# Kernel optimization log

Hardware: AMD Instinct MI355X
Metric: run time of the kernel (lower is better)

Reference implementation:

```python
import jax, jax.numpy as jnp
import numpy as np

B, S, HID = 4, 2048, 576
NH, NKV, HD = 9, 3, 64
MAXPOS, THETA = 8192, 100000.0


def rotate_half(x):
    x1, x2 = x[..., : x.shape[-1] // 2], x[..., x.shape[-1] // 2 :]
    return jnp.concatenate((-x2, x1), axis=-1)


def setup_inputs() -> dict:
    key = jax.random.key(0)
    ks = jax.random.split(key, 6)
    x = jax.random.normal(ks[0], (B, S, HID), dtype=jnp.float32)
    # RoPE tables (HuggingFace layout: freqs duplicated across halves)
    inv_freq = 1.0 / (THETA ** (np.arange(0, HD, 2, dtype=np.float32) / HD))
    freqs = np.outer(np.arange(MAXPOS, dtype=np.float32), inv_freq)
    emb = np.concatenate([freqs, freqs], axis=-1)
    cos = jnp.asarray(np.cos(emb))
    sin = jnp.asarray(np.sin(emb))
    position_ids = jnp.broadcast_to(jnp.arange(S, dtype=jnp.int64), (B, S))
    # additive causal mask [B,1,S,S]
    causal = jnp.where(
        jnp.tril(jnp.ones((S, S), dtype=bool)), 0.0, -1e9
    ).astype(jnp.float32)
    attention_mask = jnp.broadcast_to(causal, (B, 1, S, S))
    scale = 0.02
    wq = jax.random.normal(ks[1], (NH * HD, HID), dtype=jnp.float32) * scale
    wk = jax.random.normal(ks[2], (NKV * HD, HID), dtype=jnp.float32) * scale
    wv = jax.random.normal(ks[3], (NKV * HD, HID), dtype=jnp.float32) * scale
    wo = jax.random.normal(ks[4], (HID, NH * HD), dtype=jnp.float32) * scale
    return {
        "x": x, "cos": cos, "sin": sin, "position_ids": position_ids,
        "attention_mask": attention_mask,
        "wq": wq, "wk": wk, "wv": wv, "wo": wo,
    }


def reference(x, cos, sin, position_ids, attention_mask, wq, wk, wv, wo):
    b, s, _ = x.shape
    # projections (nn.Linear: y = x @ W.T), split into heads -> [B,H,S,D]
    q = (x @ wq.T).reshape(b, s, NH, HD).transpose(0, 2, 1, 3)
    k = (x @ wk.T).reshape(b, s, NKV, HD).transpose(0, 2, 1, 3)
    v = (x @ wv.T).reshape(b, s, NKV, HD).transpose(0, 2, 1, 3)
    # RoPE: cos/sin gathered per position -> [B,1,S,D], broadcast over heads
    c = cos[position_ids][:, None, :, :]
    si = sin[position_ids][:, None, :, :]
    q = q * c + rotate_half(q) * si
    k = k * c + rotate_half(k) * si
    # GQA expansion: repeat_interleave kv heads to match q heads
    k = jnp.repeat(k, NH // NKV, axis=1)
    v = jnp.repeat(v, NH // NKV, axis=1)
    scale = 1.0 / jnp.sqrt(jnp.asarray(HD, dtype=x.dtype))
    scores = jnp.einsum("bhqd,bhkd->bhqk", q, k) * scale + attention_mask
    attn = jax.nn.softmax(scores.astype(jnp.float32), axis=-1).astype(q.dtype)
    out = jnp.einsum("bhqk,bhkd->bhqd", attn, v)
    out = out.transpose(0, 2, 1, 3).reshape(b, s, NH * HD)
    return out @ wo.T
```

## Files before the change

kernel.cpp:

```cpp
#include <hip/hip_runtime.h>
#include <hip/hip_bf16.h>

#define B_    4
#define S_    2048
#define HID_  576
#define NH_   9
#define NKV_  3
#define HD_   64
#define GQ_   3

typedef __attribute__((ext_vector_type(8))) short bf16x8;
typedef __attribute__((ext_vector_type(4))) float f32x4;

__device__ __forceinline__ short f2bf(float f) {
    union { float f; unsigned int u; } v; v.f = f;
    unsigned int r = (v.u + 0x7fffu + ((v.u >> 16) & 1u)) >> 16;
    return (short)r;
}

__device__ __forceinline__ int pk2(float lo, float hi) {
    union { __hip_bfloat162 h; int u; } v;
    v.h = __float22bfloat162_rn(make_float2(lo, hi));
    return v.u;
}

__device__ __forceinline__ float exp2fast(float x) {
    return __builtin_amdgcn_exp2f(x);
}

__device__ __forceinline__ void async16(const void* g, void* l) {
    __builtin_amdgcn_global_load_lds(
        (const __attribute__((address_space(1))) unsigned int*)g,
        (__attribute__((address_space(3))) unsigned int*)l, 16, 0, 0);
}

__global__ __launch_bounds__(256) void qkv_kernel(
    const float* __restrict__ x,
    const float* __restrict__ wq,
    const float* __restrict__ wk,
    const float* __restrict__ wv,
    const float* __restrict__ cosb,
    const float* __restrict__ sinb,
    short* __restrict__ Q,
    short* __restrict__ K,
    short* __restrict__ Vt)
{
    __shared__ __align__(16) short As[2][256 * 64];
    __shared__ __align__(16) short Bs[2][64 * 64];

    const int m0     = blockIdx.x * 256;
    const int nb_blk = blockIdx.y;
    const int tid  = threadIdx.x;
    const int w    = tid >> 6, lane = tid & 63;
    const int quad = lane >> 4, c = lane & 15;
    const int lr   = lane >> 3, lg = lane & 7;
    const int sw   = lg ^ lr;
    const int xg   = quad ^ (c & 7);

    int type, head;
    if (nb_blk < NH_)            { type = 0; head = nb_blk; }
    else if (nb_blk < NH_ + NKV_){ type = 1; head = nb_blk - NH_; }
    else                         { type = 2; head = nb_blk - NH_ - NKV_; }
    const float* wsrc = (type == 0) ? wq + (size_t)head * 64 * HID_
                      : (type == 1) ? wk + (size_t)head * 64 * HID_
                                    : wv + (size_t)head * 64 * HID_;

    f32x4 acc[4][4];
    #pragma unroll
    for (int mt = 0; mt < 4; ++mt)
        #pragma unroll
        for (int nb = 0; nb < 4; ++nb) acc[mt][nb] = (f32x4){0.f, 0.f, 0.f, 0.f};

    float4 la[8][2], lb[2][2];
    auto load_stage = [&](int step) {
        const int k0 = step * 64;
        #pragma unroll
        for (int r = 0; r < 8; ++r) {
            int ch = w * 8 + r, R = ch * 8 + lr;
            const float* s = x + (size_t)(m0 + R) * HID_ + k0 + sw * 8;
            la[r][0] = *(const float4*)s;
            la[r][1] = *(const float4*)(s + 4);
        }
        #pragma unroll
        for (int r = 0; r < 2; ++r) {
            int ch = w * 2 + r, R = ch * 8 + lr;
            const float* s = wsrc + (size_t)R * HID_ + k0 + sw * 8;
            lb[r][0] = *(const float4*)s;
            lb[r][1] = *(const float4*)(s + 4);
        }
    };
    auto write_stage = [&](short* dstA, short* dstB) {
        #pragma unroll
        for (int r = 0; r < 8; ++r) {
            int ch = w * 8 + r;
            int4 p = { pk2(la[r][0].x, la[r][0].y), pk2(la[r][0].z, la[r][0].w),
                       pk2(la[r][1].x, la[r][1].y), pk2(la[r][1].z, la[r][1].w) };
            *(int4*)((char*)dstA + ch * 1024 + lane * 16) = p;
        }
        #pragma unroll
        for (int r = 0; r < 2; ++r) {
            int ch = w * 2 + r;
            int4 p = { pk2(lb[r][0].x, lb[r][0].y), pk2(lb[r][0].z, lb[r][0].w),
                       pk2(lb[r][1].x, lb[r][1].y), pk2(lb[r][1].z, lb[r][1].w) };
            *(int4*)((char*)dstB + ch * 1024 + lane * 16) = p;
        }
    };

    load_stage(0);
    write_stage(As[0], Bs[0]);

    int buf = 0;
    for (int kk = 0; kk < 9; ++kk) {
        __syncthreads();
        if (kk < 8) load_stage(kk + 1);

        const short* a_s = As[buf];
        const short* b_s = Bs[buf];
        bf16x8 bfr[4][2];
        #pragma unroll
        for (int nb = 0; nb < 4; ++nb) {
            int row = nb * 16 + c;
            bfr[nb][0] = *(const bf16x8*)(b_s + row * 64 + xg * 8);
            bfr[nb][1] = *(const bf16x8*)(b_s + row * 64 + (xg ^ 4) * 8);
        }
        #pragma unroll
        for (int mt = 0; mt < 4; ++mt) {
            int row = w * 64 + mt * 16 + c;
            bf16x8 a0 = *(const bf16x8*)(a_s + row * 64 + xg * 8);
            bf16x8 a1 = *(const bf16x8*)(a_s + row * 64 + (xg ^ 4) * 8);
            #pragma unroll
            for (int nb = 0; nb < 4; ++nb) {
                acc[mt][nb] = __builtin_amdgcn_mfma_f32_16x16x32_bf16(a0, bfr[nb][0], acc[mt][nb], 0, 0, 0);
                acc[mt][nb] = __builtin_amdgcn_mfma_f32_16x16x32_bf16(a1, bfr[nb][1], acc[mt][nb], 0, 0, 0);
            }
        }
        if (kk < 8) write_stage(As[buf ^ 1], Bs[buf ^ 1]);
        buf ^= 1;
    }

    const int b  = m0 >> 11;
    const int s0 = m0 & (S_ - 1);

    if (type < 2) {
        const float qs = (type == 0) ? 0.18033688f : 1.0f;
        #pragma unroll
        for (int mt = 0; mt < 4; ++mt)
            #pragma unroll
            for (int reg = 0; reg < 4; ++reg) {
                int s = s0 + w * 64 + mt * 16 + quad * 4 + reg;
                const float* cr = cosb + (size_t)s * HD_;
                const float* sr = sinb + (size_t)s * HD_;
                float a0 = acc[mt][0][reg], a1 = acc[mt][1][reg];
                float a2 = acc[mt][2][reg], a3 = acc[mt][3][reg];
                float o0 = (a0 * cr[c]      - a2 * sr[c])      * qs;
                float o1 = (a1 * cr[c + 16] - a3 * sr[c + 16]) * qs;
                float o2 = (a2 * cr[c + 32] + a0 * sr[c + 32]) * qs;
                float o3 = (a3 * cr[c + 48] + a1 * sr[c + 48]) * qs;
                short* dst = (type == 0)
                    ? Q + (((size_t)b * NH_  + head) * S_ + s) * HD_
                    : K + (((size_t)b * NKV_ + head) * S_ + s) * HD_;
                dst[c]      = f2bf(o0);
                dst[c + 16] = f2bf(o1);
                dst[c + 32] = f2bf(o2);
                dst[c + 48] = f2bf(o3);
            }
    } else {
        short* base = Vt + (((size_t)b * NKV_ + head) * HD_) * S_;
        #pragma unroll
        for (int mt = 0; mt < 4; ++mt) {
            int s4 = s0 + w * 64 + mt * 16 + quad * 4;
            #pragma unroll
            for (int nb = 0; nb < 4; ++nb) {
                int d = nb * 16 + c;
                short4 pk = make_short4(f2bf(acc[mt][nb][0]), f2bf(acc[mt][nb][1]),
                                        f2bf(acc[mt][nb][2]), f2bf(acc[mt][nb][3]));
                *(short4*)(base + (size_t)d * S_ + s4) = pk;
            }
        }
    }
}

#define PSTR 72

__global__ __launch_bounds__(256) void attn_kernel(
    const short* __restrict__ Q,
    const short* __restrict__ K,
    const short* __restrict__ Vt,
    short* __restrict__ AOb)
{
    __shared__ __align__(16) short Ks[2][64 * 64];
    __shared__ __align__(16) short Vs[2][64 * 64];
    __shared__ __align__(16) short Ps[3][64 * PSTR];

    const int bk = blockIdx.x;
    const int b  = bk / 3, kh = bk % 3;
    const int qt = 31 - blockIdx.y;
    const int tid  = threadIdx.x;
    const int w    = tid >> 6, lane = tid & 63;
    const int quad = lane >> 4, c = lane & 15;
    const int lr   = lane >> 3, lg = lane & 7;
    const int sw   = lg ^ lr;
    const int xg   = quad ^ (c & 7);

    const short* Kg = K  + (((size_t)b * NKV_ + kh) * S_) * HD_;
    const short* Vg = Vt + (((size_t)b * NKV_ + kh) * HD_) * S_;

    #pragma unroll
    for (int r = 0; r < 4; ++r) {
        int it = w * 4 + r;
        if (it < 8) {
            int R = it * 8 + lr;
            async16(Kg + (size_t)R * HD_ + sw * 8, (char*)Ks[0] + it * 1024);
        } else {
            int R = (it - 8) * 8 + lr;
            async16(Vg + (size_t)R * S_ + sw * 8, (char*)Vs[0] + (it - 8) * 1024);
        }
    }

    bf16x8 aq[3][2];
    #pragma unroll
    for (int hh = 0; hh < 3; ++hh) {
        const short* Qg = Q + (((size_t)b * NH_ + kh * GQ_ + hh) * S_ + qt * 64) * HD_;
        const short* qrow = Qg + (size_t)(w * 16 + c) * HD_;
        aq[hh][0] = *(const bf16x8*)(qrow + quad * 8);
        aq[hh][1] = *(const bf16x8*)(qrow + 32 + quad * 8);
    }

    bf16x8 ones;
    #pragma unroll
    for (int i = 0; i < 8; ++i) ones[i] = (short)0x3F80;

    f32x4 acc_o[3][4];
    #pragma unroll
    for (int hh = 0; hh < 3; ++hh)
        #pragma unroll
        for (int dt = 0; dt < 4; ++dt) acc_o[hh][dt] = (f32x4){0.f, 0.f, 0.f, 0.f};
    f32x4 acc_l[3] = { (f32x4){0.f,0.f,0.f,0.f}, (f32x4){0.f,0.f,0.f,0.f},
                       (f32x4){0.f,0.f,0.f,0.f} };

    auto do_tile = [&](const short* ks, const short* vs, bool MASK) {
        #pragma unroll
        for (int nb = 0; nb < 4; ++nb) {
            bf16x8 bk0 = *(const bf16x8*)(ks + (nb * 16 + c) * 64 + xg * 8);
            bf16x8 bk1 = *(const bf16x8*)(ks + (nb * 16 + c) * 64 + (xg ^ 4) * 8);
            #pragma unroll
            for (int hh = 0; hh < 3; ++hh) {
                f32x4 z = (f32x4){0.f, 0.f, 0.f, 0.f};
                z = __builtin_amdgcn_mfma_f32_16x16x32_bf16(aq[hh][0], bk0, z, 0, 0, 0);
                z = __builtin_amdgcn_mfma_f32_16x16x32_bf16(aq[hh][1], bk1, z, 0, 0, 0);
                #pragma unroll
                for (int r = 0; r < 4; ++r) {
                    float sv = z[r] - 4.0f;
                    if (MASK && (nb * 16 + c > w * 16 + quad * 4 + r)) sv = -1e30f;
                    Ps[hh][(w * 16 + quad * 4 + r) * PSTR + nb * 16 + c] = f2bf(exp2fast(sv));
                }
            }
        }
        #pragma unroll
        for (int kc = 0; kc < 2; ++kc) {
            int pg = kc ? (xg ^ 4) : xg;
            bf16x8 bv[4];
            #pragma unroll
            for (int dt = 0; dt < 4; ++dt)
                bv[dt] = *(const bf16x8*)(vs + (dt * 16 + c) * 64 + pg * 8);
            #pragma unroll
            for (int hh = 0; hh < 3; ++hh) {
                bf16x8 ap = *(const bf16x8*)(Ps[hh] + (w * 16 + c) * PSTR
                                             + quad * 8 + kc * 32);
                #pragma unroll
                for (int dt = 0; dt < 4; ++dt)
                    acc_o[hh][dt] = __builtin_amdgcn_mfma_f32_16x16x32_bf16(ap, bv[dt], acc_o[hh][dt], 0, 0, 0);
                acc_l[hh] = __builtin_amdgcn_mfma_f32_16x16x32_bf16(ap, ones, acc_l[hh], 0, 0, 0);
            }
        }
    };

    __syncthreads();

    int buf = 0;
    for (int kt = 0; kt < qt; ++kt) {
        int nxt = buf ^ 1;
        #pragma unroll
        for (int r = 0; r < 4; ++r) {
            int it = w * 4 + r;
            if (it < 8) {
                int R = it * 8 + lr;
                async16(Kg + (size_t)((kt + 1) * 64 + R) * HD_ + sw * 8,
                        (char*)Ks[nxt] + it * 1024);
            } else {
                int R = (it - 8) * 8 + lr;
                async16(Vg + (size_t)R * S_ + (kt + 1) * 64 + sw * 8,
                        (char*)Vs[nxt] + (it - 8) * 1024);
            }
        }
        do_tile(Ks[buf], Vs[buf], false);
        __syncthreads();
        buf ^= 1;
    }
    do_tile(Ks[buf], Vs[buf], true);

    #pragma unroll
    for (int hh = 0; hh < 3; ++hh)
        #pragma unroll
        for (int r = 0; r < 4; ++r) {
            int s = qt * 64 + w * 16 + quad * 4 + r;
            float inv = 1.f / acc_l[hh][r];
            short* dst = AOb + (((size_t)b * S_ + s) * NH_ + kh * GQ_ + hh) * HD_;
            #pragma unroll
            for (int dt = 0; dt < 4; ++dt)
                dst[dt * 16 + c] = f2bf(acc_o[hh][dt][r] * inv);
        }
}

__global__ __launch_bounds__(256) void oproj_kernel(
    const short* __restrict__ AOb,
    const float* __restrict__ wo,
    float* __restrict__ out)
{
    __shared__ __align__(16) short As[2][256 * 64];
    __shared__ __align__(16) short Bs[2][64 * 64];

    const int m0 = blockIdx.x * 256;
    const int n0 = blockIdx.y * 64;
    const int tid  = threadIdx.x;
    const int w    = tid >> 6, lane = tid & 63;
    const int quad = lane >> 4, c = lane & 15;
    const int lr   = lane >> 3, lg = lane & 7;
    const int sw   = lg ^ lr;
    const int xg   = quad ^ (c & 7);

    float4 lb[2][2];
    auto loadB = [&](int step) {
        const int k0 = step * 64;
        #pragma unroll
        for (int r = 0; r < 2; ++r) {
            int ch = w * 2 + r, R = ch * 8 + lr;
            const float* s = wo + (size_t)(n0 + R) * HID_ + k0 + sw * 8;
            lb[r][0] = *(const float4*)s;
            lb[r][1] = *(const float4*)(s + 4);
        }
    };
    auto writeB = [&](short* dstB) {
        #pragma unroll
        for (int r = 0; r < 2; ++r) {
            int ch = w * 2 + r;
            int4 p = { pk2(lb[r][0].x, lb[r][0].y), pk2(lb[r][0].z, lb[r][0].w),
                       pk2(lb[r][1].x, lb[r][1].y), pk2(lb[r][1].z, lb[r][1].w) };
            *(int4*)((char*)dstB + ch * 1024 + lane * 16) = p;
        }
    };
    auto stageA = [&](int step, short* dstA) {
        const int k0 = step * 64;
        #pragma unroll
        for (int r = 0; r < 8; ++r) {
            int ch = w * 8 + r, R = ch * 8 + lr;
            async16(AOb + (size_t)(m0 + R) * HID_ + k0 + sw * 8, (char*)dstA + ch * 1024);
        }
    };

    f32x4 acc[4][4];
    #pragma unroll
    for (int mt = 0; mt < 4; ++mt)
        #pragma unroll
        for (int nb = 0; nb < 4; ++nb) acc[mt][nb] = (f32x4){0.f, 0.f, 0.f, 0.f};

    stageA(0, As[0]);
    loadB(0);
    writeB(Bs[0]);

    int buf = 0;
    for (int kk = 0; kk < 9; ++kk) {
        __syncthreads();
        if (kk < 8) { stageA(kk + 1, As[buf ^ 1]); loadB(kk + 1); }

        const short* a_s = As[buf];
        const short* b_s = Bs[buf];
        bf16x8 bfr[4][2];
        #pragma unroll
        for (int nb = 0; nb < 4; ++nb) {
            int row = nb * 16 + c;
            bfr[nb][0] = *(const bf16x8*)(b_s + row * 64 + xg * 8);
            bfr[nb][1] = *(const bf16x8*)(b_s + row * 64 + (xg ^ 4) * 8);
        }
        #pragma unroll
        for (int mt = 0; mt < 4; ++mt) {
            int row = w * 64 + mt * 16 + c;
            bf16x8 a0 = *(const bf16x8*)(a_s + row * 64 + xg * 8);
            bf16x8 a1 = *(const bf16x8*)(a_s + row * 64 + (xg ^ 4) * 8);
            #pragma unroll
            for (int nb = 0; nb < 4; ++nb) {
                acc[mt][nb] = __builtin_amdgcn_mfma_f32_16x16x32_bf16(a0, bfr[nb][0], acc[mt][nb], 0, 0, 0);
                acc[mt][nb] = __builtin_amdgcn_mfma_f32_16x16x32_bf16(a1, bfr[nb][1], acc[mt][nb], 0, 0, 0);
            }
        }
        if (kk < 8) writeB(Bs[buf ^ 1]);
        buf ^= 1;
    }

    #pragma unroll
    for (int mt = 0; mt < 4; ++mt)
        #pragma unroll
        for (int reg = 0; reg < 4; ++reg) {
            int m = m0 + w * 64 + mt * 16 + quad * 4 + reg;
            float* dst = out + (size_t)m * HID_ + n0;
            #pragma unroll
            for (int nb = 0; nb < 4; ++nb)
                dst[nb * 16 + c] = acc[mt][nb][reg];
        }
}

extern "C" void kernel_launch(void* const* d_in, const int* in_sizes, int n_in,
                              void* d_out, int out_size, void* d_ws, size_t ws_size,
                              hipStream_t stream) {
    const float* x    = (const float*)d_in[0];
    const float* cosb = (const float*)d_in[1];
    const float* sinb = (const float*)d_in[2];
    const float* wq   = (const float*)d_in[5];
    const float* wk   = (const float*)d_in[6];
    const float* wv   = (const float*)d_in[7];
    const float* wo   = (const float*)d_in[8];

    short* Qb  = (short*)d_ws;
    short* Kb  = Qb  + (size_t)B_ * NH_  * S_ * HD_;
    short* Vtb = Kb  + (size_t)B_ * NKV_ * S_ * HD_;
    short* AOb = Vtb + (size_t)B_ * NKV_ * S_ * HD_;

    qkv_kernel<<<dim3(32, 15), dim3(256), 0, stream>>>(
        x, wq, wk, wv, cosb, sinb, Qb, Kb, Vtb);
    attn_kernel<<<dim3(12, 32), dim3(256), 0, stream>>>(Qb, Kb, Vtb, AOb);
    oproj_kernel<<<dim3(32, 9), dim3(256), 0, stream>>>(AOb, wo, (float*)d_out);
}
```

Before: 222.1 us.

## Split long causal query tiles across KV chunks with a separate combine kernel

```diff
diff --git a/kernel.cpp b/kernel.cpp
--- a/kernel.cpp
+++ b/kernel.cpp
@@ -17,17 +17,18 @@
     unsigned int r = (v.u + 0x7fffu + ((v.u >> 16) & 1u)) >> 16;
     return (short)r;
 }
-
+__device__ __forceinline__ float bf2f(short s) {
+    union { unsigned int u; float f; } v; v.u = ((unsigned int)(unsigned short)s) << 16;
+    return v.f;
+}
 __device__ __forceinline__ int pk2(float lo, float hi) {
     union { __hip_bfloat162 h; int u; } v;
     v.h = __float22bfloat162_rn(make_float2(lo, hi));
     return v.u;
 }
-
 __device__ __forceinline__ float exp2fast(float x) {
     return __builtin_amdgcn_exp2f(x);
 }
-
 __device__ __forceinline__ void async16(const void* g, void* l) {
     __builtin_amdgcn_global_load_lds(
         (const __attribute__((address_space(1))) unsigned int*)g,
@@ -186,7 +187,9 @@
     const short* __restrict__ Q,
     const short* __restrict__ K,
     const short* __restrict__ Vt,
-    short* __restrict__ AOb)
+    short* __restrict__ AOb,
+    short* __restrict__ Opart,
+    float* __restrict__ Lpart)
 {
     __shared__ __align__(16) short Ks[2][64 * 64];
     __shared__ __align__(16) short Vs[2][64 * 64];
@@ -194,7 +197,16 @@
 
     const int bk = blockIdx.x;
     const int b  = bk / 3, kh = bk % 3;
-    const int qt = 31 - blockIdx.y;
+    const int y  = blockIdx.y;
+    int qt, j;
+    if (y < 8)       { qt = y;                 j = 0;     }
+    else if (y < 24) { int t = y - 8;  qt = 8 + (t >> 1); j = t & 1; }
+    else if (y < 48) { int t = y - 24; qt = 16 + t / 3;   j = t % 3; }
+    else             { int t = y - 48; qt = 24 + (t >> 2); j = t & 3; }
+    const int nch = (qt >> 3) + 1;
+    const int kt0 = j * (qt + 1) / nch;
+    const int kt1 = (j + 1) * (qt + 1) / nch;
+
     const int tid  = threadIdx.x;
     const int w    = tid >> 6, lane = tid & 63;
     const int quad = lane >> 4, c = lane & 15;
@@ -210,18 +222,18 @@
         int it = w * 4 + r;
         if (it < 8) {
             int R = it * 8 + lr;
-            async16(Kg + (size_t)R * HD_ + sw * 8, (char*)Ks[0] + it * 1024);
+            async16(Kg + (size_t)(kt0 * 64 + R) * HD_ + sw * 8, (char*)Ks[0] + it * 1024);
         } else {
             int R = (it - 8) * 8 + lr;
-            async16(Vg + (size_t)R * S_ + sw * 8, (char*)Vs[0] + (it - 8) * 1024);
+            async16(Vg + (size_t)R * S_ + kt0 * 64 + sw * 8, (char*)Vs[0] + (it - 8) * 1024);
         }
     }
 
     bf16x8 aq[3][2];
     #pragma unroll
     for (int hh = 0; hh < 3; ++hh) {
-        const short* Qg = Q + (((size_t)b * NH_ + kh * GQ_ + hh) * S_ + qt * 64) * HD_;
-        const short* qrow = Qg + (size_t)(w * 16 + c) * HD_;
+        const short* qrow = Q + (((size_t)b * NH_ + kh * GQ_ + hh) * S_ + qt * 64
+                                 + w * 16 + c) * HD_;
         aq[hh][0] = *(const bf16x8*)(qrow + quad * 8);
         aq[hh][1] = *(const bf16x8*)(qrow + 32 + quad * 8);
     }
@@ -278,38 +290,92 @@
     __syncthreads();
 
     int buf = 0;
-    for (int kt = 0; kt < qt; ++kt) {
-        int nxt = buf ^ 1;
-        #pragma unroll
-        for (int r = 0; r < 4; ++r) {
-            int it = w * 4 + r;
-            if (it < 8) {
-                int R = it * 8 + lr;
-                async16(Kg + (size_t)((kt + 1) * 64 + R) * HD_ + sw * 8,
-                        (char*)Ks[nxt] + it * 1024);
-            } else {
-                int R = (it - 8) * 8 + lr;
-                async16(Vg + (size_t)R * S_ + (kt + 1) * 64 + sw * 8,
-                        (char*)Vs[nxt] + (it - 8) * 1024);
-            }
-        }
-        do_tile(Ks[buf], Vs[buf], false);
+    for (int kt = kt0; kt < kt1; ++kt) {
+        if (kt + 1 < kt1) {
+            int nxt = buf ^ 1;
+            #pragma unroll
+            for (int r = 0; r < 4; ++r) {
+                int it = w * 4 + r;
+                if (it < 8) {
+                    int R = it * 8 + lr;
+                    async16(Kg + (size_t)((kt + 1) * 64 + R) * HD_ + sw * 8,
+                            (char*)Ks[nxt] + it * 1024);
+                } else {
+                    int R = (it - 8) * 8 + lr;
+                    async16(Vg + (size_t)R * S_ + (kt + 1) * 64 + sw * 8,
+                            (char*)Vs[nxt] + (it - 8) * 1024);
+                }
+            }
+        }
+        do_tile(Ks[buf], Vs[buf], kt == qt);
         __syncthreads();
         buf ^= 1;
     }
-    do_tile(Ks[buf], Vs[buf], true);
-
-    #pragma unroll
-    for (int hh = 0; hh < 3; ++hh)
-        #pragma unroll
-        for (int r = 0; r < 4; ++r) {
-            int s = qt * 64 + w * 16 + quad * 4 + r;
-            float inv = 1.f / acc_l[hh][r];
-            short* dst = AOb + (((size_t)b * S_ + s) * NH_ + kh * GQ_ + hh) * HD_;
-            #pragma unroll
-            for (int dt = 0; dt < 4; ++dt)
-                dst[dt * 16 + c] = f2bf(acc_o[hh][dt][r] * inv);
-        }
+
+    if (nch == 1) {
+        #pragma unroll
+        for (int hh = 0; hh < 3; ++hh)
+            #pragma unroll
+            for (int r = 0; r < 4; ++r) {
+                int s = qt * 64 + w * 16 + quad * 4 + r;
+                float inv = 1.f / acc_l[hh][r];
+                short* dst = AOb + (((size_t)b * S_ + s) * NH_ + kh * GQ_ + hh) * HD_;
+                #pragma unroll
+                for (int dt = 0; dt < 4; ++dt)
+                    dst[dt * 16 + c] = f2bf(acc_o[hh][dt][r] * inv);
+            }
+    } else {
+        int off = (qt < 16) ? 2 * (qt - 8)
+                : (qt < 24) ? 16 + 3 * (qt - 16)
+                            : 40 + 4 * (qt - 24);
+        int slot = bk * 72 + off + j;
+        short* op = Opart + (size_t)slot * (3 * 64 * 64);
+        float* lp = Lpart + (size_t)slot * (3 * 64);
+        #pragma unroll
+        for (int hh = 0; hh < 3; ++hh) {
+            #pragma unroll
+            for (int r = 0; r < 4; ++r) {
+                int row = w * 16 + quad * 4 + r;
+                #pragma unroll
+                for (int dt = 0; dt < 4; ++dt)
+                    op[(hh * 64 + row) * 64 + dt * 16 + c] = f2bf(acc_o[hh][dt][r]);
+                if (c == 0) lp[hh * 64 + row] = acc_l[hh][r];
+            }
+        }
+    }
+}
+
+__global__ __launch_bounds__(256) void combine_kernel(
+    const short* __restrict__ Opart, const float* __restrict__ Lpart,
+    short* __restrict__ AOb)
+{
+    const int bk = blockIdx.x, b = bk / 3, kh = bk % 3;
+    const int qt = 8 + blockIdx.y;
+    const int nch = (qt >> 3) + 1;
+    int off = (qt < 16) ? 2 * (qt - 8)
+            : (qt < 24) ? 16 + 3 * (qt - 16)
+                        : 40 + 4 * (qt - 24);
+    const int slot0 = bk * 72 + off;
+    const int t = threadIdx.x;
+
+    __shared__ float linv[192];
+    if (t < 192) {
+        float s = 0.f;
+        for (int jj = 0; jj < nch; ++jj)
+            s += Lpart[(size_t)(slot0 + jj) * 192 + t];
+        linv[t] = 1.f / s;
+    }
+    __syncthreads();
+
+    for (int e = t; e < 3 * 64 * 64; e += 256) {
+        int hh = e >> 12, row = (e >> 6) & 63, d = e & 63;
+        float s = 0.f;
+        for (int jj = 0; jj < nch; ++jj)
+            s += bf2f(Opart[(size_t)(slot0 + jj) * 12288 + e]);
+        int sg = qt * 64 + row;
+        AOb[(((size_t)b * S_ + sg) * NH_ + kh * GQ_ + hh) * HD_ + d]
+            = f2bf(s * linv[hh * 64 + row]);
+    }
 }
 
 __global__ __launch_bounds__(256) void oproj_kernel(
@@ -420,13 +486,17 @@
     const float* wv   = (const float*)d_in[7];
     const float* wo   = (const float*)d_in[8];
 
-    short* Qb  = (short*)d_ws;
-    short* Kb  = Qb  + (size_t)B_ * NH_  * S_ * HD_;
-    short* Vtb = Kb  + (size_t)B_ * NKV_ * S_ * HD_;
-    short* AOb = Vtb + (size_t)B_ * NKV_ * S_ * HD_;
+    short* Qb    = (short*)d_ws;
+    short* Kb    = Qb  + (size_t)B_ * NH_  * S_ * HD_;
+    short* Vtb   = Kb  + (size_t)B_ * NKV_ * S_ * HD_;
+    short* AOb   = Vtb + (size_t)B_ * NKV_ * S_ * HD_;
+    short* Opart = AOb + (size_t)B_ * S_ * NH_ * HD_;
+    float* Lpart = (float*)(Opart + (size_t)864 * 3 * 64 * 64);
 
     qkv_kernel<<<dim3(32, 15), dim3(256), 0, stream>>>(
         x, wq, wk, wv, cosb, sinb, Qb, Kb, Vtb);
-    attn_kernel<<<dim3(12, 32), dim3(256), 0, stream>>>(Qb, Kb, Vtb, AOb);
+    attn_kernel<<<dim3(12, 80), dim3(256), 0, stream>>>(
+        Qb, Kb, Vtb, AOb, Opart, Lpart);
+    combine_kernel<<<dim3(12, 24), dim3(256), 0, stream>>>(Opart, Lpart, AOb);
     oproj_kernel<<<dim3(32, 9), dim3(256), 0, stream>>>(AOb, wo, (float*)d_out);
 }
```

Result: slower. 264.2 us (+19.0%).
